# Optimization experiments

Measured on AMD Instinct MI355X. Metric: run time of the kernel, lower is better.

Reference implementation:

```python
import jax, jax.numpy as jnp
import numpy as np

N_LAYERS = 8
DILATIONS = [1, 2, 1, 2, 1, 2, 1, 2]
K_HOPS = 3
BN = 13248   # batch(64) * n_nodes(207), merged as in the torch module
L = 13       # 12 history steps + 1; shrinks by sum(dilations)=12 across layers
E = 211968   # BN * avg_degree(16)


def _conv1d(x, w, b, dil):
    # x: (BN, Cin, L), w: (Cout, Cin, 2) kernel-2 dilated conv, VALID (causal shrink)
    y = jax.lax.conv_general_dilated(x, w, (1,), 'VALID', rhs_dilation=(dil,),
                                     dimension_numbers=('NCH', 'OIH', 'NCH'))
    return y + b[None, :, None]


def setup_inputs() -> dict:
    key = jax.random.key(0)
    ks = jax.random.split(key, 20)
    s = 0.1  # keep activations in a sane range
    return {
        'x': jax.random.normal(ks[0], (BN, L, 2), jnp.float32),
        'edge_src': jax.random.randint(ks[1], (E,), 0, BN),
        'edge_dst': jax.random.randint(ks[2], (E,), 0, BN),
        'edge_w': jax.random.uniform(ks[3], (E,), jnp.float32),
        'init_w': s * jax.random.normal(ks[4], (2, 32), jnp.float32),
        'init_b': s * jax.random.normal(ks[5], (32,), jnp.float32),
        'filt_w': s * jax.random.normal(ks[6], (8, 32, 32, 2), jnp.float32),
        'filt_b': s * jax.random.normal(ks[7], (8, 32), jnp.float32),
        'gate_w': s * jax.random.normal(ks[8], (8, 32, 32, 2), jnp.float32),
        'gate_b': s * jax.random.normal(ks[9], (8, 32), jnp.float32),
        'gcn_w': s * jax.random.normal(ks[10], (8, 6, 32, 32), jnp.float32),
        'gcn_b': s * jax.random.normal(ks[11], (8, 32), jnp.float32),
        'skip_w': s * jax.random.normal(ks[12], (8, 256, 32), jnp.float32),
        'skip_b': s * jax.random.normal(ks[13], (8, 256), jnp.float32),
        'out0_w': s * jax.random.normal(ks[14], (256, 512), jnp.float32),
        'out0_b': s * jax.random.normal(ks[15], (512,), jnp.float32),
        'out1_w': s * jax.random.normal(ks[16], (512, 12), jnp.float32),
        'out1_b': s * jax.random.normal(ks[17], (12,), jnp.float32),
    }


def reference(x, edge_src, edge_dst, edge_w, init_w, init_b,
              filt_w, filt_b, gate_w, gate_b, gcn_w, gcn_b,
              skip_w, skip_b, out0_w, out0_b, out1_w, out1_b):
    # init linear: (BN, L, 2) -> (BN, L, 32) -> (BN, 32, L)
    h = (x @ init_w + init_b).transpose(0, 2, 1)
    # per-hop edge weights: elementwise powers of the transition weights
    # (faithful to repo's dense_to_sparse(transition ** k)); bck = transposed edges
    adjs = [(edge_src, edge_dst, edge_w ** k) for k in range(1, K_HOPS + 1)] + \
           [(edge_dst, edge_src, edge_w ** k) for k in range(1, K_HOPS + 1)]
    skip = None
    for l in range(N_LAYERS):
        d = DILATIONS[l]
        res = h
        # Gated TCN: tanh(filter) * sigmoid(gate), seq shrinks by d
        t = jnp.tanh(_conv1d(h, filt_w[l], filt_b[l], d)) * \
            jax.nn.sigmoid(_conv1d(h, gate_w[l], gate_b[l], d))
        # Diffusion conv: sum over 6 adjacency types of A_w (x W_a)
        xt = t.transpose(0, 2, 1)  # (BN, L', 32)
        g = jnp.zeros_like(xt)
        for a, (src, dst, w) in enumerate(adjs):
            msg = (xt @ gcn_w[l, a])[src] * w[:, None, None]  # (E, L', 32)
            g = g + jax.ops.segment_sum(msg, dst, num_segments=BN)
        h = g.transpose(0, 2, 1) + gcn_b[l][None, :, None]  # (BN, 32, L')
        # residual connection (align shrunk sequence)
        h = h + res[:, :, -h.shape[-1]:]
        # skip conv (1x1) on last timestep, accumulated
        sc = h[:, :, -1] @ skip_w[l].T + skip_b[l]  # (BN, 256)
        skip = sc if skip is None else skip + sc
    out = jax.nn.relu(skip)
    out = jax.nn.relu(out @ out0_w + out0_b)
    return out @ out1_w + out1_b  # (BN, 12)
```

## Files before the change

### kernel.cpp

```cpp
#include <hip/hip_runtime.h>

#define BN 13248
#define NE 211968

typedef __attribute__((ext_vector_type(8))) short bf16x8;
typedef __attribute__((ext_vector_type(4))) float f32x4;

__device__ __forceinline__ f32x4 mfma16(bf16x8 a, bf16x8 b, f32x4 c) {
  return __builtin_amdgcn_mfma_f32_16x16x32_bf16(a, b, c, 0, 0, 0);
}

__device__ __forceinline__ unsigned short to_bf16(float v) {
  unsigned bits = __float_as_uint(v);
  return (unsigned short)((bits + 0x7FFFu + ((bits >> 16) & 1u)) >> 16);
}

__device__ __forceinline__ float fast_tanh(float x) {
  float e2 = __expf(2.f * x);
  return 1.f - 2.f / (e2 + 1.f);
}
__device__ __forceinline__ float fast_sig(float x) {
  return 1.f / (1.f + __expf(-x));
}

__global__ void k_count(const int* __restrict__ src, const int* __restrict__ dst,
                        int* __restrict__ cur_f, int* __restrict__ cur_b) {
  int e = blockIdx.x * 256 + threadIdx.x;
  if (e < NE) {
    atomicAdd(&cur_f[dst[e]], 1);
    atomicAdd(&cur_b[src[e]], 1);
  }
}

__global__ void k_scan(int* __restrict__ cur_f, int* __restrict__ row_f,
                       int* __restrict__ cur_b, int* __restrict__ row_b) {
  __shared__ int sdata[1024];
  int tid = threadIdx.x;
  for (int which = 0; which < 2; ++which) {
    int* cnt = which ? cur_b : cur_f;
    int* row = which ? row_b : row_f;
    int base = tid * 13;
    int vals[13];
    int tot = 0;
    for (int k = 0; k < 13; ++k) {
      int idx = base + k;
      int v = (idx < BN) ? cnt[idx] : 0;
      vals[k] = v; tot += v;
    }
    sdata[tid] = tot;
    __syncthreads();
    for (int off = 1; off < 1024; off <<= 1) {
      int add = (tid >= off) ? sdata[tid - off] : 0;
      __syncthreads();
      sdata[tid] += add;
      __syncthreads();
    }
    int running = sdata[tid] - tot;
    for (int k = 0; k < 13; ++k) {
      int idx = base + k;
      if (idx < BN) { row[idx] = running; cnt[idx] = running; running += vals[k]; }
    }
    if (tid == 1023) row[BN] = sdata[1023];
    __syncthreads();
  }
}

__global__ void k_fill(const int* __restrict__ src, const int* __restrict__ dst,
                       const float* __restrict__ w,
                       int* __restrict__ cur_f, int* __restrict__ col_f, float* __restrict__ w_f,
                       int* __restrict__ cur_b, int* __restrict__ col_b, float* __restrict__ w_b) {
  int e = blockIdx.x * 256 + threadIdx.x;
  if (e < NE) {
    int s = src[e], t = dst[e];
    float wv = w[e];
    int p = atomicAdd(&cur_f[t], 1); col_f[p] = s; w_f[p] = wv;
    int q = atomicAdd(&cur_b[s], 1); col_b[q] = t; w_b[q] = wv;
  }
}

__global__ void k_init(const float* __restrict__ x, const float* __restrict__ iw,
                       const float* __restrict__ ib, float* __restrict__ h) {
  int idx = blockIdx.x * 256 + threadIdx.x;
  if (idx >= BN * 13 * 32) return;
  int c = idx & 31;
  int r = idx >> 5;
  int n = r % BN;
  int tau = r / BN;
  float x0 = x[(n * 13 + tau) * 2 + 0];
  float x1 = x[(n * 13 + tau) * 2 + 1];
  h[idx] = fmaf(x0, iw[c], fmaf(x1, iw[32 + c], ib[c]));
}

__global__ void k_pack(const float* __restrict__ skip_w, const float* __restrict__ skip_b,
                       const float* __restrict__ w0, const float* __restrict__ w1,
                       const float* __restrict__ gcn_w,
                       unsigned short* __restrict__ SWb, unsigned short* __restrict__ W0T,
                       unsigned short* __restrict__ W1T, float* __restrict__ bsum,
                       unsigned short* __restrict__ GgT) {
  int id = blockIdx.x * 256 + threadIdx.x;
  if (id < 65536) {
    int j = id >> 8, k = id & 255;
    SWb[id] = to_bf16(skip_w[((k >> 5) * 256 + j) * 32 + (k & 31)]);
  }
  if (id < 131072) {
    int jo = id >> 8, k = id & 255;
    W0T[id] = to_bf16(w0[k * 512 + jo]);
  }
  if (id < 8192) {
    int n = id >> 9, k = id & 511;
    W1T[id] = (n < 12) ? to_bf16(w1[k * 12 + n]) : (unsigned short)0;
  }
  if (id < 256) {
    float s = 0.f;
    for (int l = 0; l < 8; ++l) s += skip_b[l * 256 + id];
    bsum[id] = s;
  }
  if (id < 49152) {
    int l = id / 6144, rem = id % 6144;
    int co = rem / 192, k = rem % 192;
    int a = k >> 5, ci = k & 31;
    GgT[id] = to_bf16(gcn_w[((l * 6 + a) * 32 + ci) * 32 + co]);
  }
}

template<int LIN, int D, int TPAD>
__global__ __launch_bounds__(256) void k_tcn(const float* __restrict__ h_in, unsigned short* __restrict__ t_out,
    const float* __restrict__ fw, const float* __restrict__ fb,
    const float* __restrict__ gw, const float* __restrict__ gb) {
  constexpr int LOUT = LIN - D;
  __shared__ __align__(16) float wq[32 * 32 * 4];
  __shared__ float hl[8][LIN * 32];
  int tid = threadIdx.x;
  for (int f = tid; f < 4096; f += 256) {
    int e = f & 3, co = (f >> 2) & 31, ci = f >> 7;
    const float* srcw = (e < 2) ? fw : gw;
    wq[f] = srcw[(co * 32 + ci) * 2 + (e & 1)];
  }
  int n0 = blockIdx.x * 8;
  for (int i = tid; i < 8 * LIN * 32; i += 256) {
    int c = i & 31, r = i >> 5;
    int nl = r / LIN, tau = r % LIN;
    hl[nl][tau * 32 + c] = h_in[(tau * BN + n0 + nl) * 32 + c];
  }
  __syncthreads();
  int nl = tid >> 5, co = tid & 31;
  int n = n0 + nl;
  float accf[LOUT], accg[LOUT];
  float fbv = fb[co], gbv = gb[co];
#pragma unroll
  for (int j = 0; j < LOUT; ++j) { accf[j] = fbv; accg[j] = gbv; }
#pragma unroll
  for (int ci = 0; ci < 32; ++ci) {
    float4 wv = *(const float4*)&wq[(ci * 32 + co) * 4];
    float xr[LIN];
#pragma unroll
    for (int t = 0; t < LIN; ++t) xr[t] = hl[nl][t * 32 + ci];
#pragma unroll
    for (int j = 0; j < LOUT; ++j) {
      accf[j] = fmaf(xr[j], wv.x, accf[j]);
      accf[j] = fmaf(xr[j + D], wv.y, accf[j]);
      accg[j] = fmaf(xr[j], wv.z, accg[j]);
      accg[j] = fmaf(xr[j + D], wv.w, accg[j]);
    }
  }
#pragma unroll
  for (int j = 0; j < LOUT; ++j) {
    float v = fast_tanh(accf[j]) * fast_sig(accg[j]);
    t_out[(n * TPAD + j) * 32 + co] = to_bf16(v);
  }
}

__device__ __forceinline__ void bf4_fma(uint2 u, float w1, float4* A) {
  float v0 = __uint_as_float(u.x << 16);
  float v1 = __uint_as_float(u.x & 0xFFFF0000u);
  float v2 = __uint_as_float(u.y << 16);
  float v3 = __uint_as_float(u.y & 0xFFFF0000u);
  float w2 = w1 * w1, w3 = w2 * w1;
  A[0].x = fmaf(w1, v0, A[0].x); A[0].y = fmaf(w1, v1, A[0].y);
  A[0].z = fmaf(w1, v2, A[0].z); A[0].w = fmaf(w1, v3, A[0].w);
  A[1].x = fmaf(w2, v0, A[1].x); A[1].y = fmaf(w2, v1, A[1].y);
  A[1].z = fmaf(w2, v2, A[1].z); A[1].w = fmaf(w2, v3, A[1].w);
  A[2].x = fmaf(w3, v0, A[2].x); A[2].y = fmaf(w3, v1, A[2].y);
  A[2].z = fmaf(w3, v2, A[2].z); A[2].w = fmaf(w3, v3, A[2].w);
}

template<int TPAD>
__device__ __forceinline__ void gather_dir(const unsigned short* __restrict__ t_in,
    int e0, int e1, const int* __restrict__ col, const float* __restrict__ warr,
    int lane32, int rowoff, float4* A) {
  for (int base = e0; base < e1; base += 32) {
    int idx = base + lane32;
    int cv = 0; float wv = 0.f;
    if (idx < e1) { cv = col[idx]; wv = warr[idx]; }
    int cnt = min(32, e1 - base);
    int b = 0;
    for (; b + 8 <= cnt; b += 8) {
      uint2 u[8]; float w1[8];
#pragma unroll
      for (int k = 0; k < 8; ++k) {
        int s = __shfl(cv, b + k, 32);
        w1[k] = __shfl(wv, b + k, 32);
        u[k] = *(const uint2*)(t_in + s * (TPAD * 32) + rowoff);
      }
#pragma unroll
      for (int k = 0; k < 8; ++k) bf4_fma(u[k], w1[k], A);
    }
    for (; b < cnt; ++b) {
      int s = __shfl(cv, b, 32);
      float ww = __shfl(wv, b, 32);
      uint2 u = *(const uint2*)(t_in + s * (TPAD * 32) + rowoff);
      bf4_fma(u, ww, A);
    }
  }
}

#define ZSTRIDE 200

template<int LOUT, int D, int TPAD>
__global__ __launch_bounds__(256) void k_agg(const unsigned short* __restrict__ t_in,
    const float* __restrict__ h_in, float* __restrict__ h_out, float* __restrict__ lastcol,
    const int* __restrict__ row_f, const int* __restrict__ col_f, const float* __restrict__ w_f,
    const int* __restrict__ row_b, const int* __restrict__ col_b, const float* __restrict__ w_b,
    const unsigned short* __restrict__ WgT,
    const float* __restrict__ bias) {
  __shared__ __align__(16) unsigned short Zl[32 * ZSTRIDE];
  int tid = threadIdx.x;
  int nl = tid >> 5, lane32 = tid & 31;
  int tl = lane32 >> 3;
  int c4 = (lane32 & 7) << 2;
  int n = blockIdx.x * 8 + nl;
  int tau0 = blockIdx.y * 4;
  int rowoff = (tau0 + tl) * 32 + c4;
  int ef0 = row_f[n], ef1 = row_f[n + 1];
  int eb0 = row_b[n], eb1 = row_b[n + 1];
  float4 acc[6];
#pragma unroll
  for (int a = 0; a < 6; ++a) acc[a] = make_float4(0.f, 0.f, 0.f, 0.f);
  gather_dir<TPAD>(t_in, ef0, ef1, col_f, w_f, lane32, rowoff, acc + 0);
  gather_dir<TPAD>(t_in, eb0, eb1, col_b, w_b, lane32, rowoff, acc + 3);
  int m = nl * 4 + tl;
#pragma unroll
  for (int a = 0; a < 6; ++a) {
    ushort4 pk;
    pk.x = to_bf16(acc[a].x); pk.y = to_bf16(acc[a].y);
    pk.z = to_bf16(acc[a].z); pk.w = to_bf16(acc[a].w);
    *(ushort4*)(&Zl[m * ZSTRIDE + a * 32 + c4]) = pk;
  }
  __syncthreads();
  int wave = tid >> 6, lane = tid & 63;
  int m16 = lane & 15, q = lane >> 4;
  int mt = wave >> 1, nt = wave & 1;
  f32x4 dacc = (f32x4){0.f, 0.f, 0.f, 0.f};
#pragma unroll
  for (int ks = 0; ks < 6; ++ks) {
    bf16x8 av = *(const bf16x8*)(&Zl[(mt * 16 + m16) * ZSTRIDE + ks * 32 + q * 8]);
    bf16x8 bv = *(const bf16x8*)(WgT + (nt * 16 + m16) * 192 + ks * 32 + q * 8);
    dacc = mfma16(av, bv, dacc);
  }
  int co = nt * 16 + m16;
  float bco = bias[co];
#pragma unroll
  for (int r = 0; r < 4; ++r) {
    int mm = mt * 16 + q * 4 + r;
    int node = blockIdx.x * 8 + (mm >> 2);
    int tau = tau0 + (mm & 3);
    if (tau < LOUT) {
      float rres = h_in[((tau + D) * BN + node) * 32 + co];
      float o = dacc[r] + bco + rres;
      h_out[(tau * BN + node) * 32 + co] = o;
      if (tau == LOUT - 1) lastcol[node * 32 + co] = o;
    }
  }
}

__device__ __forceinline__ bf16x8 ldsA(const unsigned short* buf, int stride, int row, int ks, int q) {
  int unit = ks * 4 + q;
  int addr = row * stride + ((unit ^ (row & 7)) << 3);
  return *(const bf16x8*)(buf + addr);
}

__global__ __launch_bounds__(256) void k_final(const float* __restrict__ lastcol,
    const unsigned short* __restrict__ SWb, const unsigned short* __restrict__ W0T,
    const unsigned short* __restrict__ W1T, const float* __restrict__ bsum,
    const float* __restrict__ b0, const float* __restrict__ b1,
    float* __restrict__ out) {
  __shared__ __align__(16) unsigned short Z[32 * 256];
  __shared__ __align__(16) unsigned short H[32 * 512];
  int tid = threadIdx.x;
  int wave = tid >> 6, lane = tid & 63;
  int m16 = lane & 15, q = lane >> 4;
  int n0 = blockIdx.x * 32;
#pragma unroll
  for (int it = 0; it < 32; ++it) {
    int id = it * 256 + tid;
    int m = id >> 8, k = id & 255;
    float v = lastcol[((k >> 5) * BN + n0 + m) * 32 + (k & 31)];
    Z[m * 256 + (((k >> 3) ^ (m & 7)) << 3) + (k & 7)] = to_bf16(v);
  }
  __syncthreads();
  f32x4 acc1[2][4];
#pragma unroll
  for (int mt = 0; mt < 2; ++mt)
#pragma unroll
    for (int i = 0; i < 4; ++i) acc1[mt][i] = (f32x4){0.f, 0.f, 0.f, 0.f};
#pragma unroll
  for (int ks = 0; ks < 8; ++ks) {
    bf16x8 a0 = ldsA(Z, 256, m16, ks, q);
    bf16x8 a1 = ldsA(Z, 256, 16 + m16, ks, q);
#pragma unroll
    for (int i = 0; i < 4; ++i) {
      int j = (wave * 4 + i) * 16 + m16;
      bf16x8 b = *(const bf16x8*)(SWb + j * 256 + ks * 32 + q * 8);
      acc1[0][i] = mfma16(a0, b, acc1[0][i]);
      acc1[1][i] = mfma16(a1, b, acc1[1][i]);
    }
  }
  __syncthreads();
#pragma unroll
  for (int i = 0; i < 4; ++i) {
    int j = (wave * 4 + i) * 16 + m16;
    float bs = bsum[j];
#pragma unroll
    for (int mt = 0; mt < 2; ++mt)
#pragma unroll
      for (int r = 0; r < 4; ++r) {
        int row = mt * 16 + q * 4 + r;
        float v = fmaxf(acc1[mt][i][r] + bs, 0.f);
        Z[row * 256 + (((j >> 3) ^ (row & 7)) << 3) + (j & 7)] = to_bf16(v);
      }
  }
  __syncthreads();
  f32x4 acc2[2][8];
#pragma unroll
  for (int mt = 0; mt < 2; ++mt)
#pragma unroll
    for (int i = 0; i < 8; ++i) acc2[mt][i] = (f32x4){0.f, 0.f, 0.f, 0.f};
#pragma unroll
  for (int ks = 0; ks < 8; ++ks) {
    bf16x8 a0 = ldsA(Z, 256, m16, ks, q);
    bf16x8 a1 = ldsA(Z, 256, 16 + m16, ks, q);
#pragma unroll
    for (int i = 0; i < 8; ++i) {
      int jo = (wave * 8 + i) * 16 + m16;
      bf16x8 b = *(const bf16x8*)(W0T + jo * 256 + ks * 32 + q * 8);
      acc2[0][i] = mfma16(a0, b, acc2[0][i]);
      acc2[1][i] = mfma16(a1, b, acc2[1][i]);
    }
  }
#pragma unroll
  for (int i = 0; i < 8; ++i) {
    int jo = (wave * 8 + i) * 16 + m16;
    float b0v = b0[jo];
#pragma unroll
    for (int mt = 0; mt < 2; ++mt)
#pragma unroll
      for (int r = 0; r < 4; ++r) {
        int row = mt * 16 + q * 4 + r;
        float v = fmaxf(acc2[mt][i][r] + b0v, 0.f);
        H[row * 512 + (((jo >> 3) ^ (row & 7)) << 3) + (jo & 7)] = to_bf16(v);
      }
  }
  __syncthreads();
  if (wave < 2) {
    f32x4 acc3 = (f32x4){0.f, 0.f, 0.f, 0.f};
#pragma unroll
    for (int ks = 0; ks < 16; ++ks) {
      bf16x8 a = ldsA(H, 512, wave * 16 + m16, ks, q);
      bf16x8 b = *(const bf16x8*)(W1T + m16 * 512 + ks * 32 + q * 8);
      acc3 = mfma16(a, b, acc3);
    }
    if (m16 < 12) {
      float bv = b1[m16];
#pragma unroll
      for (int r = 0; r < 4; ++r)
        out[(n0 + wave * 16 + q * 4 + r) * 12 + m16] = acc3[r] + bv;
    }
  }
}

extern "C" void kernel_launch(void* const* d_in, const int* in_sizes, int n_in,
                              void* d_out, int out_size, void* d_ws, size_t ws_size,
                              hipStream_t stream) {
  const float* x      = (const float*)d_in[0];
  const int*   esrc   = (const int*)d_in[1];
  const int*   edst   = (const int*)d_in[2];
  const float* ew     = (const float*)d_in[3];
  const float* init_w = (const float*)d_in[4];
  const float* init_b = (const float*)d_in[5];
  const float* filt_w = (const float*)d_in[6];
  const float* filt_b = (const float*)d_in[7];
  const float* gate_w = (const float*)d_in[8];
  const float* gate_b = (const float*)d_in[9];
  const float* gcn_w  = (const float*)d_in[10];
  const float* gcn_b  = (const float*)d_in[11];
  const float* skip_w = (const float*)d_in[12];
  const float* skip_b = (const float*)d_in[13];
  const float* w0     = (const float*)d_in[14];
  const float* b0     = (const float*)d_in[15];
  const float* w1     = (const float*)d_in[16];
  const float* b1     = (const float*)d_in[17];
  float* out = (float*)d_out;

  float* base = (float*)d_ws;
  float* hA      = base;
  float* hB      = hA + 13 * BN * 32;
  float* tbuf    = hB + 13 * BN * 32;
  float* lastcol = tbuf + 12 * BN * 32;
  int* row_f = (int*)(lastcol + 8 * BN * 32);
  int* row_b = row_f + (BN + 1);
  int* cur_f = row_b + (BN + 1);
  int* cur_b = cur_f + BN;
  int* col_f = cur_b + BN;
  int* col_b = col_f + NE;
  float* wgt_f = (float*)(col_b + NE);
  float* wgt_b = wgt_f + NE;
  unsigned short* tbuf_u = (unsigned short*)tbuf;
  unsigned short* SWb = tbuf_u + 16 * BN * 32;
  unsigned short* W0T = SWb + 65536;
  unsigned short* W1T = W0T + 131072;
  float* bsumv = (float*)(W1T + 8192);
  unsigned short* GgT = (unsigned short*)(bsumv + 256);

  hipMemsetAsync(cur_f, 0, 2 * BN * sizeof(int), stream);
  const int egrid = (NE + 255) / 256;
  k_count<<<egrid, 256, 0, stream>>>(esrc, edst, cur_f, cur_b);
  k_scan<<<1, 1024, 0, stream>>>(cur_f, row_f, cur_b, row_b);
  k_fill<<<egrid, 256, 0, stream>>>(esrc, edst, ew, cur_f, col_f, wgt_f, cur_b, col_b, wgt_b);
  k_init<<<(BN * 13 * 32 + 255) / 256, 256, 0, stream>>>(x, init_w, init_b, hA);
  k_pack<<<512, 256, 0, stream>>>(skip_w, skip_b, w0, w1, gcn_w, SWb, W0T, W1T, bsumv, GgT);

  const int ngrid = BN / 8;
#define LAYER(l, LIN, DD, TP, hin, hout) \
  k_tcn<LIN, DD, TP><<<ngrid, 256, 0, stream>>>(hin, tbuf_u, filt_w + l * 2048, filt_b + l * 32, \
                                                gate_w + l * 2048, gate_b + l * 32); \
  k_agg<LIN - DD, DD, TP><<<dim3(ngrid, ((LIN - DD) + 3) / 4), 256, 0, stream>>>(tbuf_u, hin, hout, \
      lastcol + l * BN * 32, row_f, col_f, wgt_f, row_b, col_b, wgt_b, GgT + l * 6144, gcn_b + l * 32);

  LAYER(0, 13, 1, 12, hA, hB)
  LAYER(1, 12, 2, 12, hB, hA)
  LAYER(2, 10, 1, 12, hA, hB)
  LAYER(3,  9, 2, 12, hB, hA)
  LAYER(4,  7, 1,  8, hA, hB)
  LAYER(5,  6, 2,  8, hB, hA)
  LAYER(6,  4, 1,  4, hA, hB)
  LAYER(7,  3, 2,  4, hB, hA)
#undef LAYER

  k_final<<<BN / 32, 256, 0, stream>>>(lastcol, SWb, W0T, W1T, bsumv, b0, b1, out);
}
```

Baseline: 762.2 us.

## Process all timesteps per block in graph aggregation to reuse edge index loads

```diff
diff --git a/kernel.cpp b/kernel.cpp
--- a/kernel.cpp
+++ b/kernel.cpp
@@ -164,52 +164,64 @@
     }
   }
 #pragma unroll
-  for (int j = 0; j < LOUT; ++j) {
-    float v = fast_tanh(accf[j]) * fast_sig(accg[j]);
-    t_out[(n * TPAD + j) * 32 + co] = to_bf16(v);
-  }
-}
-
-__device__ __forceinline__ void bf4_fma(uint2 u, float w1, float4* A) {
+  for (int j = 0; j < TPAD; ++j) {
+    float v = (j < LOUT) ? fast_tanh(accf[j < LOUT ? j : 0]) * fast_sig(accg[j < LOUT ? j : 0]) : 0.f;
+    t_out[(n * TPAD + j) * 32 + co] = (j < LOUT) ? to_bf16(v) : (unsigned short)0;
+  }
+}
+
+__device__ __forceinline__ void bf4_fma3(uint2 u, float w1, float w2, float w3,
+                                         float4* A0, float4* A1, float4* A2) {
   float v0 = __uint_as_float(u.x << 16);
   float v1 = __uint_as_float(u.x & 0xFFFF0000u);
   float v2 = __uint_as_float(u.y << 16);
   float v3 = __uint_as_float(u.y & 0xFFFF0000u);
-  float w2 = w1 * w1, w3 = w2 * w1;
-  A[0].x = fmaf(w1, v0, A[0].x); A[0].y = fmaf(w1, v1, A[0].y);
-  A[0].z = fmaf(w1, v2, A[0].z); A[0].w = fmaf(w1, v3, A[0].w);
-  A[1].x = fmaf(w2, v0, A[1].x); A[1].y = fmaf(w2, v1, A[1].y);
-  A[1].z = fmaf(w2, v2, A[1].z); A[1].w = fmaf(w2, v3, A[1].w);
-  A[2].x = fmaf(w3, v0, A[2].x); A[2].y = fmaf(w3, v1, A[2].y);
-  A[2].z = fmaf(w3, v2, A[2].z); A[2].w = fmaf(w3, v3, A[2].w);
-}
-
-template<int TPAD>
+  A0->x = fmaf(w1, v0, A0->x); A0->y = fmaf(w1, v1, A0->y);
+  A0->z = fmaf(w1, v2, A0->z); A0->w = fmaf(w1, v3, A0->w);
+  A1->x = fmaf(w2, v0, A1->x); A1->y = fmaf(w2, v1, A1->y);
+  A1->z = fmaf(w2, v2, A1->z); A1->w = fmaf(w2, v3, A1->w);
+  A2->x = fmaf(w3, v0, A2->x); A2->y = fmaf(w3, v1, A2->y);
+  A2->z = fmaf(w3, v2, A2->z); A2->w = fmaf(w3, v3, A2->w);
+}
+
+template<int TPAD, int NT>
 __device__ __forceinline__ void gather_dir(const unsigned short* __restrict__ t_in,
     int e0, int e1, const int* __restrict__ col, const float* __restrict__ warr,
-    int lane32, int rowoff, float4* A) {
+    int lane32, int rowoff0, float4 (*A)[NT]) {
   for (int base = e0; base < e1; base += 32) {
     int idx = base + lane32;
     int cv = 0; float wv = 0.f;
     if (idx < e1) { cv = col[idx]; wv = warr[idx]; }
     int cnt = min(32, e1 - base);
     int b = 0;
-    for (; b + 8 <= cnt; b += 8) {
-      uint2 u[8]; float w1[8];
-#pragma unroll
-      for (int k = 0; k < 8; ++k) {
+    for (; b + 4 <= cnt; b += 4) {
+      uint2 u[4][NT]; float w1[4];
+#pragma unroll
+      for (int k = 0; k < 4; ++k) {
         int s = __shfl(cv, b + k, 32);
         w1[k] = __shfl(wv, b + k, 32);
-        u[k] = *(const uint2*)(t_in + s * (TPAD * 32) + rowoff);
-      }
-#pragma unroll
-      for (int k = 0; k < 8; ++k) bf4_fma(u[k], w1[k], A);
+        const unsigned short* p = t_in + s * (TPAD * 32) + rowoff0;
+#pragma unroll
+        for (int j = 0; j < NT; ++j) u[k][j] = *(const uint2*)(p + j * 32);
+      }
+#pragma unroll
+      for (int k = 0; k < 4; ++k) {
+        float w2 = w1[k] * w1[k], w3 = w2 * w1[k];
+#pragma unroll
+        for (int j = 0; j < NT; ++j)
+          bf4_fma3(u[k][j], w1[k], w2, w3, &A[0][j], &A[1][j], &A[2][j]);
+      }
     }
     for (; b < cnt; ++b) {
       int s = __shfl(cv, b, 32);
       float ww = __shfl(wv, b, 32);
-      uint2 u = *(const uint2*)(t_in + s * (TPAD * 32) + rowoff);
-      bf4_fma(u, ww, A);
+      float w2 = ww * ww, w3 = w2 * ww;
+      const unsigned short* p = t_in + s * (TPAD * 32) + rowoff0;
+#pragma unroll
+      for (int j = 0; j < NT; ++j) {
+        uint2 u = *(const uint2*)(p + j * 32);
+        bf4_fma3(u, ww, w2, w3, &A[0][j], &A[1][j], &A[2][j]);
+      }
     }
   }
 }
@@ -217,58 +229,74 @@
 #define ZSTRIDE 200
 
 template<int LOUT, int D, int TPAD>
-__global__ __launch_bounds__(256) void k_agg(const unsigned short* __restrict__ t_in,
+__global__ __launch_bounds__(256, 3) void k_agg(const unsigned short* __restrict__ t_in,
     const float* __restrict__ h_in, float* __restrict__ h_out, float* __restrict__ lastcol,
     const int* __restrict__ row_f, const int* __restrict__ col_f, const float* __restrict__ w_f,
     const int* __restrict__ row_b, const int* __restrict__ col_b, const float* __restrict__ w_b,
     const unsigned short* __restrict__ WgT,
     const float* __restrict__ bias) {
-  __shared__ __align__(16) unsigned short Zl[32 * ZSTRIDE];
+  constexpr int NT = TPAD / 4;
+  __shared__ __align__(16) unsigned short Zl[8 * TPAD * ZSTRIDE];
   int tid = threadIdx.x;
   int nl = tid >> 5, lane32 = tid & 31;
   int tl = lane32 >> 3;
   int c4 = (lane32 & 7) << 2;
-  int n = blockIdx.x * 8 + nl;
-  int tau0 = blockIdx.y * 4;
-  int rowoff = (tau0 + tl) * 32 + c4;
+  int n0 = blockIdx.x * 8;
+  int n = n0 + nl;
+  int rowoff0 = (tl * NT) * 32 + c4;
   int ef0 = row_f[n], ef1 = row_f[n + 1];
   int eb0 = row_b[n], eb1 = row_b[n + 1];
-  float4 acc[6];
-#pragma unroll
-  for (int a = 0; a < 6; ++a) acc[a] = make_float4(0.f, 0.f, 0.f, 0.f);
-  gather_dir<TPAD>(t_in, ef0, ef1, col_f, w_f, lane32, rowoff, acc + 0);
-  gather_dir<TPAD>(t_in, eb0, eb1, col_b, w_b, lane32, rowoff, acc + 3);
-  int m = nl * 4 + tl;
-#pragma unroll
-  for (int a = 0; a < 6; ++a) {
-    ushort4 pk;
-    pk.x = to_bf16(acc[a].x); pk.y = to_bf16(acc[a].y);
-    pk.z = to_bf16(acc[a].z); pk.w = to_bf16(acc[a].w);
-    *(ushort4*)(&Zl[m * ZSTRIDE + a * 32 + c4]) = pk;
+  float4 accf[3][NT], accb[3][NT];
+#pragma unroll
+  for (int a = 0; a < 3; ++a)
+#pragma unroll
+    for (int j = 0; j < NT; ++j) {
+      accf[a][j] = make_float4(0.f, 0.f, 0.f, 0.f);
+      accb[a][j] = make_float4(0.f, 0.f, 0.f, 0.f);
+    }
+  gather_dir<TPAD, NT>(t_in, ef0, ef1, col_f, w_f, lane32, rowoff0, accf);
+  gather_dir<TPAD, NT>(t_in, eb0, eb1, col_b, w_b, lane32, rowoff0, accb);
+#pragma unroll
+  for (int j = 0; j < NT; ++j) {
+    int m = nl * TPAD + tl * NT + j;
+#pragma unroll
+    for (int a = 0; a < 3; ++a) {
+      ushort4 pf, pb;
+      pf.x = to_bf16(accf[a][j].x); pf.y = to_bf16(accf[a][j].y);
+      pf.z = to_bf16(accf[a][j].z); pf.w = to_bf16(accf[a][j].w);
+      pb.x = to_bf16(accb[a][j].x); pb.y = to_bf16(accb[a][j].y);
+      pb.z = to_bf16(accb[a][j].z); pb.w = to_bf16(accb[a][j].w);
+      *(ushort4*)(&Zl[m * ZSTRIDE + a * 32 + c4]) = pf;
+      *(ushort4*)(&Zl[m * ZSTRIDE + (a + 3) * 32 + c4]) = pb;
+    }
   }
   __syncthreads();
   int wave = tid >> 6, lane = tid & 63;
   int m16 = lane & 15, q = lane >> 4;
-  int mt = wave >> 1, nt = wave & 1;
-  f32x4 dacc = (f32x4){0.f, 0.f, 0.f, 0.f};
-#pragma unroll
-  for (int ks = 0; ks < 6; ++ks) {
-    bf16x8 av = *(const bf16x8*)(&Zl[(mt * 16 + m16) * ZSTRIDE + ks * 32 + q * 8]);
-    bf16x8 bv = *(const bf16x8*)(WgT + (nt * 16 + m16) * 192 + ks * 32 + q * 8);
-    dacc = mfma16(av, bv, dacc);
-  }
-  int co = nt * 16 + m16;
-  float bco = bias[co];
-#pragma unroll
-  for (int r = 0; r < 4; ++r) {
-    int mm = mt * 16 + q * 4 + r;
-    int node = blockIdx.x * 8 + (mm >> 2);
-    int tau = tau0 + (mm & 3);
-    if (tau < LOUT) {
-      float rres = h_in[((tau + D) * BN + node) * 32 + co];
-      float o = dacc[r] + bco + rres;
-      h_out[(tau * BN + node) * 32 + co] = o;
-      if (tau == LOUT - 1) lastcol[node * 32 + co] = o;
+#pragma unroll
+  for (int i = 0; i < NT; ++i) {
+    int u = wave * NT + i;
+    int mt = u >> 1, nt = u & 1;
+    f32x4 dacc = (f32x4){0.f, 0.f, 0.f, 0.f};
+#pragma unroll
+    for (int ks = 0; ks < 6; ++ks) {
+      bf16x8 av = *(const bf16x8*)(&Zl[(mt * 16 + m16) * ZSTRIDE + ks * 32 + q * 8]);
+      bf16x8 bv = *(const bf16x8*)(WgT + (nt * 16 + m16) * 192 + ks * 32 + q * 8);
+      dacc = mfma16(av, bv, dacc);
+    }
+    int co = nt * 16 + m16;
+    float bco = bias[co];
+#pragma unroll
+    for (int r = 0; r < 4; ++r) {
+      int mm = mt * 16 + q * 4 + r;
+      int node = n0 + mm / TPAD;
+      int tau = mm % TPAD;
+      if (tau < LOUT) {
+        float rres = h_in[((tau + D) * BN + node) * 32 + co];
+        float o = dacc[r] + bco + rres;
+        h_out[(tau * BN + node) * 32 + co] = o;
+        if (tau == LOUT - 1) lastcol[node * 32 + co] = o;
+      }
     }
   }
 }
@@ -433,15 +461,15 @@
 #define LAYER(l, LIN, DD, TP, hin, hout) \
   k_tcn<LIN, DD, TP><<<ngrid, 256, 0, stream>>>(hin, tbuf_u, filt_w + l * 2048, filt_b + l * 32, \
                                                 gate_w + l * 2048, gate_b + l * 32); \
-  k_agg<LIN - DD, DD, TP><<<dim3(ngrid, ((LIN - DD) + 3) / 4), 256, 0, stream>>>(tbuf_u, hin, hout, \
+  k_agg<LIN - DD, DD, TP><<<ngrid, 256, 0, stream>>>(tbuf_u, hin, hout, \
       lastcol + l * BN * 32, row_f, col_f, wgt_f, row_b, col_b, wgt_b, GgT + l * 6144, gcn_b + l * 32);
 
   LAYER(0, 13, 1, 12, hA, hB)
   LAYER(1, 12, 2, 12, hB, hA)
   LAYER(2, 10, 1, 12, hA, hB)
-  LAYER(3,  9, 2, 12, hB, hA)
+  LAYER(3,  9, 2,  8, hB, hA)
   LAYER(4,  7, 1,  8, hA, hB)
-  LAYER(5,  6, 2,  8, hB, hA)
+  LAYER(5,  6, 2,  4, hB, hA)
   LAYER(6,  4, 1,  4, hA, hB)
   LAYER(7,  3, 2,  4, hB, hA)
 #undef LAYER
```

New measurement: 758.7 us. No clear change (-0.5%).
